# Kernel optimization log

Hardware: AMD Instinct MI355X
Metric: run time of the kernel (lower is better)

The kernel has to match this reference:

```python
import jax, jax.numpy as jnp
import numpy as np

IOU_HI = 0.5
IOU_LO = 0.0
ROI_BS = 256
POS_RATIO = 0.25
BG = 20  # background class id; valid classes 0..BG-1
NUM_POS = int(ROI_BS * POS_RATIO)
DELTAS_SCALING = np.array([10.0, 10.0, 5.0, 5.0], dtype=np.float32)  # (x, y, w, h)


def _make_boxes(key, shape):
    ka, kb = jax.random.split(key)
    c = jax.random.uniform(ka, shape + (2,), minval=0.05, maxval=0.95)
    s = jax.random.uniform(kb, shape + (2,), minval=0.02, maxval=0.4)
    lo = jnp.clip(c - s / 2, 0.0, 1.0)
    hi = jnp.clip(c + s / 2, 0.0, 1.0)
    return jnp.concatenate([lo, hi], -1)  # (y1, x1, y2, x2), normalized


def setup_inputs() -> dict:
    key = jax.random.key(0)
    k1, k2, k3 = jax.random.split(key, 3)
    B, N, G = 32, 12000, 200
    rois = _make_boxes(k1, (B, N))
    gt_boxes = _make_boxes(k2, (B, G))
    # class == BG marks a padded / invalid GT box
    gt_class_ids = jax.random.randint(k3, (B, G), 0, BG + 1).astype(jnp.int32)
    return {"rois": rois, "gt_class_ids": gt_class_ids, "gt_boxes": gt_boxes}


def _iou(rois, gts):
    # rois [N,4], gts [G,4] in (y1,x1,y2,x2) -> [N,G]
    y1 = jnp.maximum(rois[:, None, 0], gts[None, :, 0])
    x1 = jnp.maximum(rois[:, None, 1], gts[None, :, 1])
    y2 = jnp.minimum(rois[:, None, 2], gts[None, :, 2])
    x2 = jnp.minimum(rois[:, None, 3], gts[None, :, 3])
    inter = jnp.clip(y2 - y1, 0.0) * jnp.clip(x2 - x1, 0.0)
    ar = (rois[:, 2] - rois[:, 0]) * (rois[:, 3] - rois[:, 1])
    ag = (gts[:, 2] - gts[:, 0]) * (gts[:, 3] - gts[:, 1])
    return inter / (ar[:, None] + ag[None, :] - inter + 1e-8)


def _encode(r, g):
    # (tx, ty, tw, th) * scaling, r/g: [K,4] in (y1,x1,y2,x2)
    eps = 1e-6
    rh = r[:, 2] - r[:, 0]; rw = r[:, 3] - r[:, 1]
    rcy = r[:, 0] + rh / 2; rcx = r[:, 1] + rw / 2
    gh = g[:, 2] - g[:, 0]; gw = g[:, 3] - g[:, 1]
    gcy = g[:, 0] + gh / 2; gcx = g[:, 1] + gw / 2
    tx = (gcx - rcx) / (rw + eps)
    ty = (gcy - rcy) / (rh + eps)
    tw = jnp.log(jnp.maximum(gw, eps) / (rw + eps))
    th = jnp.log(jnp.maximum(gh, eps) / (rh + eps))
    return jnp.stack([tx, ty, tw, th], -1) * jnp.asarray(DELTAS_SCALING)


def _per_image(rois, gt_cls, gt_boxes):
    iou = _iou(rois, gt_boxes)                       # [N,G]
    valid_gt = gt_cls < BG
    iou = jnp.where(valid_gt[None, :], iou, -1.0)
    max_iou = iou.max(1)                             # [N]
    best_gt = iou.argmax(1)                          # [N]
    pos = max_iou >= IOU_HI
    neg = (max_iou < IOU_HI) & (max_iou >= IOU_LO)

    # deterministic sampling: highest-IoU positives / negatives first
    pos_val, pos_idx = jax.lax.top_k(jnp.where(pos, max_iou, -1.0), NUM_POS)
    pos_ok = pos_val > 0.0
    neg_val, neg_idx = jax.lax.top_k(jnp.where(neg, max_iou + 2.0, -1.0), ROI_BS)
    neg_ok = neg_val > 0.0

    rP = jnp.arange(NUM_POS, dtype=jnp.float32)
    rN = jnp.arange(ROI_BS, dtype=jnp.float32)
    prio = jnp.concatenate([jnp.where(pos_ok, 1e9 - rP, -1e9 - rP),
                            jnp.where(neg_ok, 1e6 - rN, -1e6 - rN)])
    cand_idx = jnp.concatenate([pos_idx, neg_idx])
    cand_pos = jnp.concatenate([pos_ok, jnp.zeros(ROI_BS, bool)])
    _, sel = jax.lax.top_k(prio, ROI_BS)
    sel_roi = cand_idx[sel]                          # [ROI_BS]
    sel_is_pos = cand_pos[sel]                       # [ROI_BS]

    labels = jnp.where(sel_is_pos, gt_cls[best_gt[sel_roi]], BG)
    rois_sel = rois[sel_roi]                         # [ROI_BS,4]
    gts_sel = gt_boxes[best_gt[sel_roi]]             # [ROI_BS,4]
    t = _encode(rois_sel, gts_sel) * sel_is_pos[:, None].astype(rois.dtype)

    cls_onehot = jax.nn.one_hot(labels, BG + 1, dtype=rois.dtype)   # [ROI_BS,BG+1]
    onehot_fg = jax.nn.one_hot(labels, BG, dtype=rois.dtype)        # zero row for bg
    mask4 = jnp.repeat(onehot_fg, 4, axis=1)                        # [ROI_BS,4*BG]
    deltas_full = (onehot_fg[:, :, None] * t[:, None, :]).reshape(ROI_BS, 4 * BG)
    reg = jnp.concatenate([mask4, deltas_full], -1)                 # [ROI_BS,8*BG]
    return rois_sel, cls_onehot, reg


def reference(rois, gt_class_ids, gt_boxes):
    return jax.vmap(_per_image)(rois, gt_class_ids, gt_boxes)
```

## Files before the change

### kernel.cpp

```cpp
#include <hip/hip_runtime.h>
#include <stdint.h>

#pragma clang fp contract(off)

#define BATCH 32
#define NROI  12000
#define NGT   200
#define BGCLS 20
#define ROIBS 256
#define NPOS  64
#define NBIN  1024
#define CAP   1024
#define TSEL  1024
#define VPT2  12
#define HSH   16
#define HST   (NBIN + 2)
#define RPT   2
#define IOBLK (256 * RPT)

__device__ __forceinline__ void roi_maxiou_all(const float4* cbox, const float* carea,
                                               int nv, float ry1, float rx1,
                                               float ry2, float rx2,
                                               float& best, int& bj) {
#pragma clang fp contract(off)
  float ar = (ry2 - ry1) * (rx2 - rx1);
  best = -1.0f; bj = 0;
  for (int j = 0; j < nv; ++j) {
    float4 q = cbox[j];
    float yy1 = fmaxf(ry1, q.x);
    float xx1 = fmaxf(rx1, q.y);
    float yy2 = fminf(ry2, q.z);
    float xx2 = fminf(rx2, q.w);
    float inter = fmaxf(yy2 - yy1, 0.0f) * fmaxf(xx2 - xx1, 0.0f);
    float den = ((ar + carea[j]) - inter) + 1e-8f;
    float iou = inter / den;
    if (iou > best) { best = iou; bj = j; }
  }
}

__global__ __launch_bounds__(256, 4) void k_ioumax(const float* __restrict__ rois,
                                                   const int* __restrict__ gtc,
                                                   const float* __restrict__ gtb,
                                                   float* __restrict__ max_iou,
                                                   int* __restrict__ best_j) {
#pragma clang fp contract(off)
  __shared__ float4 cbox[NGT];
  __shared__ float carea[NGT];
  __shared__ int snv, wtmp[4];
  const int b = blockIdx.y;
  const int tid = threadIdx.x;

  {
    bool valid = false; float4 p = make_float4(0.f, 0.f, 0.f, 0.f);
    if (tid < NGT) {
      p = *(const float4*)(gtb + ((size_t)b * NGT + tid) * 4);
      valid = gtc[(size_t)b * NGT + tid] < BGCLS;
    }
    unsigned long long m = __ballot(valid);
    int w = tid >> 6;
    if ((tid & 63) == 0) wtmp[w] = __popcll(m);
    __syncthreads();
    if (tid == 0) snv = wtmp[0] + wtmp[1] + wtmp[2] + wtmp[3];
    if (valid) {
      int off = 0;
      for (int i = 0; i < w; ++i) off += wtmp[i];
      int pos = off + __popcll(m & ((1ull << (tid & 63)) - 1ull));
      cbox[pos] = p;
      carea[pos] = (p.z - p.x) * (p.w - p.y);
    }
    __syncthreads();
  }
  const int nv = snv;
  const int n0 = blockIdx.x * IOBLK + tid;

  float4 rb[RPT]; float ar[RPT]; float v1[RPT], v2[RPT]; int j1[RPT];
#pragma unroll
  for (int k = 0; k < RPT; ++k) {
    int n = n0 + (k << 8);
    rb[k] = (n < NROI) ? *(const float4*)(rois + ((size_t)b * NROI + n) * 4)
                       : make_float4(2.f, 2.f, 2.f, 2.f);
    ar[k] = (rb[k].z - rb[k].x) * (rb[k].w - rb[k].y);
    v1[k] = -1.0f; v2[k] = -2.0f; j1[k] = 0;
  }
#pragma unroll 2
  for (int j = 0; j < nv; ++j) {
    float4 q = cbox[j];
    float ag = carea[j];
#pragma unroll
    for (int k = 0; k < RPT; ++k) {
      float yy1 = fmaxf(rb[k].x, q.x);
      float xx1 = fmaxf(rb[k].y, q.y);
      float yy2 = fminf(rb[k].z, q.z);
      float xx2 = fminf(rb[k].w, q.w);
      float inter = fmaxf(yy2 - yy1, 0.0f) * fmaxf(xx2 - xx1, 0.0f);
      float den = ((ar[k] + ag) - inter) + 1e-8f;
      float a = inter * __builtin_amdgcn_rcpf(den);
      bool gt = a > v1[k];
      v2[k] = gt ? v1[k] : fmaxf(v2[k], a);
      j1[k] = gt ? j : j1[k];
      v1[k] = gt ? a : v1[k];
    }
  }
#pragma unroll
  for (int k = 0; k < RPT; ++k) {
    int n = n0 + (k << 8);
    if (n >= NROI) continue;
    float best; int bj;
    if (nv == 0) {
      best = -1.0f; bj = 0;
    } else if (v2[k] >= v1[k] * 0.999995f) {
      roi_maxiou_all(cbox, carea, nv, rb[k].x, rb[k].y, rb[k].z, rb[k].w, best, bj);
    } else {
      float4 q = cbox[j1[k]];
      float yy1 = fmaxf(rb[k].x, q.x);
      float xx1 = fmaxf(rb[k].y, q.y);
      float yy2 = fminf(rb[k].z, q.z);
      float xx2 = fminf(rb[k].w, q.w);
      float inter = fmaxf(yy2 - yy1, 0.0f) * fmaxf(xx2 - xx1, 0.0f);
      float den = ((ar[k] + carea[j1[k]]) - inter) + 1e-8f;
      best = inter / den;
      bj = j1[k];
    }
    max_iou[(size_t)b * NROI + n] = best;
    best_j[(size_t)b * NROI + n] = bj;
  }
}

template <bool USE_WS>
__global__ __launch_bounds__(TSEL) void k_sel(const float* __restrict__ rois,
                                              const int* __restrict__ gtc,
                                              const float* __restrict__ gtb,
                                              const float* __restrict__ max_iou,
                                              const int* __restrict__ best_j,
                                              float* __restrict__ out) {
#pragma clang fp contract(off)
  __shared__ float4 cbox[NGT];
  __shared__ float carea[NGT];
  __shared__ int ccls[NGT];
  __shared__ int snv, wtmp[16];
  __shared__ int wtot[16], wnext[16];
  __shared__ unsigned long long list[CAP];
  __shared__ int hs[HSH][HST];
  __shared__ int ss[NBIN];
  __shared__ int sel_r[ROIBS];
  __shared__ int scnt, sT;
  const int b = blockIdx.x;
  const int tid = threadIdx.x;
  const int lane = tid & 63;

  {
    bool valid = false; float4 p = make_float4(0.f, 0.f, 0.f, 0.f); int cls = BGCLS;
    if (tid < NGT) {
      p = *(const float4*)(gtb + ((size_t)b * NGT + tid) * 4);
      cls = gtc[(size_t)b * NGT + tid];
      valid = (cls < BGCLS);
    }
    unsigned long long m = __ballot(valid);
    int w = tid >> 6;
    if ((tid & 63) == 0) wtmp[w] = __popcll(m);
    if (tid < ROIBS) sel_r[tid] = 0;
    __syncthreads();
    if (tid == 0) { int s = 0; for (int i = 0; i < 16; ++i) s += wtmp[i]; snv = s; }
    if (valid) {
      int off = 0;
      for (int i = 0; i < w; ++i) off += wtmp[i];
      int pos = off + __popcll(m & ((1ull << (tid & 63)) - 1ull));
      cbox[pos] = p;
      carea[pos] = (p.z - p.x) * (p.w - p.y);
      ccls[pos] = cls;
    }
    __syncthreads();
  }
  const int nv = snv;

  float v[VPT2];
#pragma unroll
  for (int i = 0; i < VPT2; ++i) {
    int n = tid + (i << 10);
    if constexpr (USE_WS) {
      v[i] = (n < NROI) ? max_iou[(size_t)b * NROI + n] : -3.0f;
    } else {
      if (n < NROI) {
        const float4 r = *(const float4*)(rois + ((size_t)b * NROI + n) * 4);
        float best; int bj;
        roi_maxiou_all(cbox, carea, nv, r.x, r.y, r.z, r.w, best, bj);
        v[i] = best;
      } else v[i] = -3.0f;
    }
  }

  auto phase = [&](bool isPos, int need, unsigned base, int shift,
                   float lo, float hi, int slotBase) -> int {
    for (int i = tid; i < HSH * HST; i += TSEL) ((int*)hs)[i] = 0;
    if (tid == 0) { scnt = 0; sT = 0; }
    __syncthreads();
    const int sh = tid & (HSH - 1);
#pragma unroll
    for (int i = 0; i < VPT2; ++i) {
      float x = v[i];
      if (x >= lo && x < hi) {
        float kv = isPos ? x : (x + 2.0f);
        int bin = min((int)((__float_as_uint(kv) - base) >> shift), NBIN - 1);
        atomicAdd(&hs[sh][bin], 1);
      }
    }
    __syncthreads();
    int cnt_bin = 0;
#pragma unroll
    for (int i = 0; i < HSH; ++i) cnt_bin += hs[i][tid];
    const int w = tid >> 6;
    int sfx = cnt_bin;
#pragma unroll
    for (int off = 1; off < 64; off <<= 1) {
      int t = __shfl_down(sfx, off, 64);
      sfx += (lane + off < 64) ? t : 0;
    }
    if (lane == 0) wtot[w] = sfx;
    __syncthreads();
    if (tid < 16) {
      int s = 0;
      for (int i = tid + 1; i < 16; ++i) s += wtot[i];
      wnext[tid] = s;
    }
    __syncthreads();
    const int suffix = sfx + wnext[w];
    ss[tid] = suffix;
    __syncthreads();
    {
      int nxt = (tid + 1 < NBIN) ? ss[tid + 1] : 0;
      if (suffix >= need && nxt < need) sT = tid;
    }
    __syncthreads();
    const int T = sT;
#pragma unroll
    for (int i = 0; i < VPT2; ++i) {
      int n = tid + (i << 10);
      float x = v[i];
      bool pred = (x >= lo && x < hi);
      unsigned kh = 0; 
      if (pred) {
        kh = __float_as_uint(isPos ? x : (x + 2.0f));
        int bin = min((int)((kh - base) >> shift), NBIN - 1);
        pred = (bin >= T);
      }
      unsigned long long mk = __ballot(pred);
      int c = __popcll(mk);
      int bs = 0;
      if (lane == 0 && c) bs = atomicAdd(&scnt, c);
      bs = __shfl(bs, 0, 64);
      if (pred) {
        int idx = bs + __popcll(mk & ((1ull << lane) - 1ull));
        if (idx < CAP)
          list[idx] = ((unsigned long long)kh << 32) | (unsigned)(0x7fffffff - n);
      }
    }
    __syncthreads();
    const int cnt = min(scnt, CAP);
    const int limit = min(cnt, need);
    if (tid < cnt) {
      unsigned long long ki = list[tid];
      int rank = 0;
      for (int j = 0; j < cnt; ++j) rank += (list[j] > ki);
      if (rank < limit)
        sel_r[slotBase + rank] = 0x7fffffff - (int)(ki & 0xffffffffu);
    }
    __syncthreads();
    return limit;
  };

  const int P = phase(true, NPOS, 0x3F000000u, 13, 0.5f, 3.0f, 0);
  phase(false, ROIBS - P, 0x40000000u, 11, 0.0f, 0.5f, P);

  {
    const int slot = tid >> 2, q = tid & 3;
    const int r = sel_r[slot];
    const int isp = (slot < P) ? 1 : 0;
    const float4 rv = *(const float4*)(rois + ((size_t)b * NROI + r) * 4);
    float ry1 = rv.x, rx1 = rv.y, ry2 = rv.z, rx2 = rv.w;
    int bj;
    if constexpr (USE_WS) {
      bj = best_j[(size_t)b * NROI + r];
    } else {
      float bb;
      roi_maxiou_all(cbox, carea, nv, ry1, rx1, ry2, rx2, bb, bj);
    }
    int label = isp ? ccls[bj] : BGCLS;

    float* out1 = out;
    float* out2 = out + (size_t)BATCH * ROIBS * 4;
    float* out3 = out + (size_t)BATCH * ROIBS * 25;
    size_t row = (size_t)b * ROIBS + slot;

    if (q == 0) {
      *(float4*)(out1 + row * 4) = rv;
      float* o2 = out2 + row * 21;
      for (int c = 0; c <= BGCLS; ++c) o2[c] = (c == label) ? 1.0f : 0.0f;
    }

    float t0 = 0.f, t1 = 0.f, t2 = 0.f, t3 = 0.f;
    if (isp) {
      const float eps = 1e-6f;
      float4 g = cbox[bj];
      float gy1 = g.x, gx1 = g.y, gy2 = g.z, gx2 = g.w;
      float rh = ry2 - ry1, rw = rx2 - rx1;
      float rcy = ry1 + rh * 0.5f, rcx = rx1 + rw * 0.5f;
      float gh = gy2 - gy1, gw = gx2 - gx1;
      float gcy = gy1 + gh * 0.5f, gcx = gx1 + gw * 0.5f;
      t0 = ((gcx - rcx) / (rw + eps)) * 10.0f;
      t1 = ((gcy - rcy) / (rh + eps)) * 10.0f;
      t2 = logf(fmaxf(gw, eps) / (rw + eps)) * 5.0f;
      t3 = logf(fmaxf(gh, eps) / (rh + eps)) * 5.0f;
    }
    int m0 = label * 4;
    float* o3 = out3 + row * 160;
    for (int c = q * 10; c < q * 10 + 10; ++c) {
      float4 wv = make_float4(0.f, 0.f, 0.f, 0.f);
      if (isp) {
        float* wp = &wv.x;
#pragma unroll
        for (int jj = 0; jj < 4; ++jj) {
          int e = c * 4 + jj;
          float x = 0.f;
          if (e >= m0 && e < m0 + 4) x = 1.0f;
          int d = e - 80 - m0;
          if (d == 0) x = t0; else if (d == 1) x = t1;
          else if (d == 2) x = t2; else if (d == 3) x = t3;
          wp[jj] = x;
        }
      }
      *(float4*)(o3 + c * 4) = wv;
    }
  }
}

extern "C" void kernel_launch(void* const* d_in, const int* in_sizes, int n_in,
                              void* d_out, int out_size, void* d_ws, size_t ws_size,
                              hipStream_t stream) {
  const float* rois = (const float*)d_in[0];
  const int*   gtc  = (const int*)d_in[1];
  const float* gtb  = (const float*)d_in[2];
  float*       out  = (float*)d_out;

  size_t need = (size_t)BATCH * NROI * 8;
  if (d_ws && ws_size >= need) {
    float* mi = (float*)d_ws;
    int*   bj = (int*)d_ws + (size_t)BATCH * NROI;
    k_ioumax<<<dim3((NROI + IOBLK - 1) / IOBLK, BATCH), 256, 0, stream>>>(rois, gtc, gtb, mi, bj);
    k_sel<true><<<BATCH, TSEL, 0, stream>>>(rois, gtc, gtb, mi, bj, out);
  } else {
    k_sel<false><<<BATCH, TSEL, 0, stream>>>(rois, gtc, gtb, nullptr, nullptr, out);
  }
}
```

Measured before the change: 89.53 us.

## Use approximate max-IoU prefilter, recompute exact IoU only for boundary candidates

The first kernel now computes only an approximate max IoU per ROI, using a fast reciprocal and a two-way max. It no longer tracks the argmax or runs exact fallbacks, and it stops writing the best_j array. The selection kernel picks candidates with a widened margin around the 0.5 threshold and lowered histogram cutoffs, then recomputes exact IoU and argmax for those candidates only before ranking. This removes the per-ROI argmax bookkeeping and half the workspace traffic. In exchange it adds exact recomputation in the single-block-per-image selection kernel and a larger candidate buffer, and it relies on the margin to keep results exact.

```diff
diff --git a/kernel.cpp b/kernel.cpp
--- a/kernel.cpp
+++ b/kernel.cpp
@@ -10,13 +10,12 @@
 #define ROIBS 256
 #define NPOS  64
 #define NBIN  1024
-#define CAP   1024
+#define CAP   2048
 #define TSEL  1024
 #define VPT2  12
 #define HSH   16
 #define HST   (NBIN + 2)
-#define RPT   2
-#define IOBLK (256 * RPT)
+#define DELTA 1e-6f
 
 __device__ __forceinline__ void roi_maxiou_all(const float4* cbox, const float* carea,
                                                int nv, float ry1, float rx1,
@@ -38,12 +37,29 @@
   }
 }
 
-__global__ __launch_bounds__(256, 4) void k_ioumax(const float* __restrict__ rois,
-                                                   const int* __restrict__ gtc,
-                                                   const float* __restrict__ gtb,
-                                                   float* __restrict__ max_iou,
-                                                   int* __restrict__ best_j) {
-#pragma clang fp contract(off)
+__device__ __forceinline__ float approx_max(const float4* cbox, const float* carea,
+                                            int nv, float4 r) {
+  float ar = (r.z - r.x) * (r.w - r.y);
+  float va = -1.0f, vb = -1.0f;
+#pragma unroll 4
+  for (int j = 0; j < nv; ++j) {
+    float4 q = cbox[j];
+    float yy1 = fmaxf(r.x, q.x);
+    float xx1 = fmaxf(r.y, q.y);
+    float yy2 = fminf(r.z, q.z);
+    float xx2 = fminf(r.w, q.w);
+    float inter = fmaxf(yy2 - yy1, 0.0f) * fmaxf(xx2 - xx1, 0.0f);
+    float den = ((ar + carea[j]) - inter) + 1e-8f;
+    float a = inter * __builtin_amdgcn_rcpf(den);
+    if (j & 1) vb = fmaxf(vb, a); else va = fmaxf(va, a);
+  }
+  return fmaxf(va, vb);
+}
+
+__global__ __launch_bounds__(256) void k_ioumax(const float* __restrict__ rois,
+                                                const int* __restrict__ gtc,
+                                                const float* __restrict__ gtb,
+                                                float* __restrict__ max_iou) {
   __shared__ float4 cbox[NGT];
   __shared__ float carea[NGT];
   __shared__ int snv, wtmp[4];
@@ -70,60 +86,10 @@
     }
     __syncthreads();
   }
-  const int nv = snv;
-  const int n0 = blockIdx.x * IOBLK + tid;
-
-  float4 rb[RPT]; float ar[RPT]; float v1[RPT], v2[RPT]; int j1[RPT];
-#pragma unroll
-  for (int k = 0; k < RPT; ++k) {
-    int n = n0 + (k << 8);
-    rb[k] = (n < NROI) ? *(const float4*)(rois + ((size_t)b * NROI + n) * 4)
-                       : make_float4(2.f, 2.f, 2.f, 2.f);
-    ar[k] = (rb[k].z - rb[k].x) * (rb[k].w - rb[k].y);
-    v1[k] = -1.0f; v2[k] = -2.0f; j1[k] = 0;
-  }
-#pragma unroll 2
-  for (int j = 0; j < nv; ++j) {
-    float4 q = cbox[j];
-    float ag = carea[j];
-#pragma unroll
-    for (int k = 0; k < RPT; ++k) {
-      float yy1 = fmaxf(rb[k].x, q.x);
-      float xx1 = fmaxf(rb[k].y, q.y);
-      float yy2 = fminf(rb[k].z, q.z);
-      float xx2 = fminf(rb[k].w, q.w);
-      float inter = fmaxf(yy2 - yy1, 0.0f) * fmaxf(xx2 - xx1, 0.0f);
-      float den = ((ar[k] + ag) - inter) + 1e-8f;
-      float a = inter * __builtin_amdgcn_rcpf(den);
-      bool gt = a > v1[k];
-      v2[k] = gt ? v1[k] : fmaxf(v2[k], a);
-      j1[k] = gt ? j : j1[k];
-      v1[k] = gt ? a : v1[k];
-    }
-  }
-#pragma unroll
-  for (int k = 0; k < RPT; ++k) {
-    int n = n0 + (k << 8);
-    if (n >= NROI) continue;
-    float best; int bj;
-    if (nv == 0) {
-      best = -1.0f; bj = 0;
-    } else if (v2[k] >= v1[k] * 0.999995f) {
-      roi_maxiou_all(cbox, carea, nv, rb[k].x, rb[k].y, rb[k].z, rb[k].w, best, bj);
-    } else {
-      float4 q = cbox[j1[k]];
-      float yy1 = fmaxf(rb[k].x, q.x);
-      float xx1 = fmaxf(rb[k].y, q.y);
-      float yy2 = fminf(rb[k].z, q.z);
-      float xx2 = fminf(rb[k].w, q.w);
-      float inter = fmaxf(yy2 - yy1, 0.0f) * fmaxf(xx2 - xx1, 0.0f);
-      float den = ((ar[k] + carea[j1[k]]) - inter) + 1e-8f;
-      best = inter / den;
-      bj = j1[k];
-    }
-    max_iou[(size_t)b * NROI + n] = best;
-    best_j[(size_t)b * NROI + n] = bj;
-  }
+  int n = blockIdx.x * 256 + tid;
+  if (n >= NROI) return;
+  const float4 r = *(const float4*)(rois + ((size_t)b * NROI + n) * 4);
+  max_iou[(size_t)b * NROI + n] = approx_max(cbox, carea, snv, r);
 }
 
 template <bool USE_WS>
@@ -131,7 +97,6 @@
                                               const int* __restrict__ gtc,
                                               const float* __restrict__ gtb,
                                               const float* __restrict__ max_iou,
-                                              const int* __restrict__ best_j,
                                               float* __restrict__ out) {
 #pragma clang fp contract(off)
   __shared__ float4 cbox[NGT];
@@ -139,11 +104,14 @@
   __shared__ int ccls[NGT];
   __shared__ int snv, wtmp[16];
   __shared__ int wtot[16], wnext[16];
-  __shared__ unsigned long long list[CAP];
+  __shared__ int plist[CAP];
+  __shared__ unsigned long long keyl[CAP];
+  __shared__ int bjl[CAP];
   __shared__ int hs[HSH][HST];
   __shared__ int ss[NBIN];
   __shared__ int sel_r[ROIBS];
-  __shared__ int scnt, sT;
+  __shared__ int sel_b[ROIBS];
+  __shared__ int scnt, sX, sT, sPos;
   const int b = blockIdx.x;
   const int tid = threadIdx.x;
   const int lane = tid & 63;
@@ -158,7 +126,7 @@
     unsigned long long m = __ballot(valid);
     int w = tid >> 6;
     if ((tid & 63) == 0) wtmp[w] = __popcll(m);
-    if (tid < ROIBS) sel_r[tid] = 0;
+    if (tid < ROIBS) { sel_r[tid] = 0; sel_b[tid] = 0; }
     __syncthreads();
     if (tid == 0) { int s = 0; for (int i = 0; i < 16; ++i) s += wtmp[i]; snv = s; }
     if (valid) {
@@ -177,33 +145,23 @@
 #pragma unroll
   for (int i = 0; i < VPT2; ++i) {
     int n = tid + (i << 10);
-    if constexpr (USE_WS) {
-      v[i] = (n < NROI) ? max_iou[(size_t)b * NROI + n] : -3.0f;
-    } else {
-      if (n < NROI) {
+    if (n < NROI) {
+      if constexpr (USE_WS) {
+        v[i] = max_iou[(size_t)b * NROI + n];
+      } else {
         const float4 r = *(const float4*)(rois + ((size_t)b * NROI + n) * 4);
-        float best; int bj;
-        roi_maxiou_all(cbox, carea, nv, r.x, r.y, r.z, r.w, best, bj);
-        v[i] = best;
-      } else v[i] = -3.0f;
-    }
-  }
-
-  auto phase = [&](bool isPos, int need, unsigned base, int shift,
-                   float lo, float hi, int slotBase) -> int {
-    for (int i = tid; i < HSH * HST; i += TSEL) ((int*)hs)[i] = 0;
-    if (tid == 0) { scnt = 0; sT = 0; }
-    __syncthreads();
-    const int sh = tid & (HSH - 1);
-#pragma unroll
-    for (int i = 0; i < VPT2; ++i) {
-      float x = v[i];
-      if (x >= lo && x < hi) {
-        float kv = isPos ? x : (x + 2.0f);
-        int bin = min((int)((__float_as_uint(kv) - base) >> shift), NBIN - 1);
-        atomicAdd(&hs[sh][bin], 1);
+        v[i] = approx_max(cbox, carea, nv, r);
       }
-    }
+    } else v[i] = -3.0f;
+  }
+
+  auto mkbin = [](unsigned kh, unsigned base, int shift) -> int {
+    int bin = ((int)(kh - base)) >> shift;
+    return max(min(bin, NBIN - 1), 0);
+  };
+
+  auto find_T = [&](int needv) -> int {
+    if (tid == 0) sT = 0;
     __syncthreads();
     int cnt_bin = 0;
 #pragma unroll
@@ -226,64 +184,136 @@
     const int suffix = sfx + wnext[w];
     ss[tid] = suffix;
     __syncthreads();
-    {
-      int nxt = (tid + 1 < NBIN) ? ss[tid + 1] : 0;
-      if (suffix >= need && nxt < need) sT = tid;
-    }
-    __syncthreads();
-    const int T = sT;
-#pragma unroll
-    for (int i = 0; i < VPT2; ++i) {
-      int n = tid + (i << 10);
-      float x = v[i];
-      bool pred = (x >= lo && x < hi);
-      unsigned kh = 0; 
-      if (pred) {
-        kh = __float_as_uint(isPos ? x : (x + 2.0f));
-        int bin = min((int)((kh - base) >> shift), NBIN - 1);
-        pred = (bin >= T);
+    int nxt = (tid + 1 < NBIN) ? ss[tid + 1] : 0;
+    if (suffix >= needv && nxt < needv) sT = tid;
+    __syncthreads();
+    return sT;
+  };
+
+  const int sh = tid & (HSH - 1);
+
+  for (int i = tid; i < HSH * HST; i += TSEL) ((int*)hs)[i] = 0;
+  if (tid == 0) { scnt = 0; sX = 0; sPos = 0; }
+  __syncthreads();
+#pragma unroll
+  for (int i = 0; i < VPT2; ++i) {
+    int n = tid + (i << 10);
+    float x = v[i];
+    bool inb = (n < NROI) && (x >= 0.5f - DELTA);
+    if (inb) atomicAdd(&hs[sh][mkbin(__float_as_uint(x), 0x3F000000u, 13)], 1);
+    bool bnd = inb && (x < 0.5f + DELTA);
+    unsigned long long mx = __ballot(bnd);
+    if (lane == 0 && mx) atomicAdd(&sX, __popcll(mx));
+  }
+  __syncthreads();
+  const int XB = sX;
+  const int Tp = max(find_T(NPOS + XB) - 2, 0);
+#pragma unroll
+  for (int i = 0; i < VPT2; ++i) {
+    int n = tid + (i << 10);
+    float x = v[i];
+    bool pred = (n < NROI) && (x >= 0.5f - DELTA) &&
+                (mkbin(__float_as_uint(x), 0x3F000000u, 13) >= Tp);
+    unsigned long long mk = __ballot(pred);
+    int c = __popcll(mk);
+    int bs = 0;
+    if (lane == 0 && c) bs = atomicAdd(&scnt, c);
+    bs = __shfl(bs, 0, 64);
+    if (pred) {
+      int idx = bs + __popcll(mk & ((1ull << lane) - 1ull));
+      if (idx < CAP) plist[idx] = n;
+    }
+  }
+  __syncthreads();
+  const int cntp = min(scnt, CAP);
+  for (int i = tid; i < cntp; i += TSEL) {
+    int n = plist[i];
+    const float4 r = *(const float4*)(rois + ((size_t)b * NROI + n) * 4);
+    float best; int bj;
+    roi_maxiou_all(cbox, carea, nv, r.x, r.y, r.z, r.w, best, bj);
+    bool ok = (best >= 0.5f);
+    keyl[i] = ok ? (((unsigned long long)__float_as_uint(best) << 32)
+                   | (unsigned)(0x7fffffff - n)) : 0ull;
+    bjl[i] = bj;
+    if (ok) atomicAdd(&sPos, 1);
+  }
+  __syncthreads();
+  const int P = min(sPos, NPOS);
+  for (int i = tid; i < cntp; i += TSEL) {
+    unsigned long long ki = keyl[i];
+    if (ki) {
+      int rank = 0;
+      for (int j = 0; j < cntp; ++j) rank += (keyl[j] > ki);
+      if (rank < P) {
+        sel_r[rank] = 0x7fffffff - (int)(ki & 0xffffffffu);
+        sel_b[rank] = bjl[i];
       }
-      unsigned long long mk = __ballot(pred);
-      int c = __popcll(mk);
-      int bs = 0;
-      if (lane == 0 && c) bs = atomicAdd(&scnt, c);
-      bs = __shfl(bs, 0, 64);
-      if (pred) {
-        int idx = bs + __popcll(mk & ((1ull << lane) - 1ull));
-        if (idx < CAP)
-          list[idx] = ((unsigned long long)kh << 32) | (unsigned)(0x7fffffff - n);
+    }
+  }
+  __syncthreads();
+
+  const int need = ROIBS - P;
+  for (int i = tid; i < HSH * HST; i += TSEL) ((int*)hs)[i] = 0;
+  if (tid == 0) scnt = 0;
+  __syncthreads();
+#pragma unroll
+  for (int i = 0; i < VPT2; ++i) {
+    int n = tid + (i << 10);
+    float x = v[i];
+    if (n < NROI && x < 0.5f + DELTA)
+      atomicAdd(&hs[sh][mkbin(__float_as_uint(x + 2.0f), 0x40000000u, 11)], 1);
+  }
+  __syncthreads();
+  const int Tn = max(find_T(need + XB) - 2, 0);
+#pragma unroll
+  for (int i = 0; i < VPT2; ++i) {
+    int n = tid + (i << 10);
+    float x = v[i];
+    bool pred = (n < NROI) && (x < 0.5f + DELTA) &&
+                (mkbin(__float_as_uint(x + 2.0f), 0x40000000u, 11) >= Tn);
+    unsigned long long mk = __ballot(pred);
+    int c = __popcll(mk);
+    int bs = 0;
+    if (lane == 0 && c) bs = atomicAdd(&scnt, c);
+    bs = __shfl(bs, 0, 64);
+    if (pred) {
+      int idx = bs + __popcll(mk & ((1ull << lane) - 1ull));
+      if (idx < CAP) plist[idx] = n;
+    }
+  }
+  __syncthreads();
+  const int cntn = min(scnt, CAP);
+  for (int i = tid; i < cntn; i += TSEL) {
+    int n = plist[i];
+    const float4 r = *(const float4*)(rois + ((size_t)b * NROI + n) * 4);
+    float best; int bj;
+    roi_maxiou_all(cbox, carea, nv, r.x, r.y, r.z, r.w, best, bj);
+    bool ok = (best < 0.5f);
+    keyl[i] = ok ? (((unsigned long long)__float_as_uint(best + 2.0f) << 32)
+                   | (unsigned)(0x7fffffff - n)) : 0ull;
+    bjl[i] = bj;
+  }
+  __syncthreads();
+  for (int i = tid; i < cntn; i += TSEL) {
+    unsigned long long ki = keyl[i];
+    if (ki) {
+      int rank = 0;
+      for (int j = 0; j < cntn; ++j) rank += (keyl[j] > ki);
+      if (rank < need) {
+        sel_r[P + rank] = 0x7fffffff - (int)(ki & 0xffffffffu);
+        sel_b[P + rank] = bjl[i];
       }
     }
-    __syncthreads();
-    const int cnt = min(scnt, CAP);
-    const int limit = min(cnt, need);
-    if (tid < cnt) {
-      unsigned long long ki = list[tid];
-      int rank = 0;
-      for (int j = 0; j < cnt; ++j) rank += (list[j] > ki);
-      if (rank < limit)
-        sel_r[slotBase + rank] = 0x7fffffff - (int)(ki & 0xffffffffu);
-    }
-    __syncthreads();
-    return limit;
-  };
-
-  const int P = phase(true, NPOS, 0x3F000000u, 13, 0.5f, 3.0f, 0);
-  phase(false, ROIBS - P, 0x40000000u, 11, 0.0f, 0.5f, P);
+  }
+  __syncthreads();
 
   {
     const int slot = tid >> 2, q = tid & 3;
     const int r = sel_r[slot];
+    const int bj = sel_b[slot];
     const int isp = (slot < P) ? 1 : 0;
     const float4 rv = *(const float4*)(rois + ((size_t)b * NROI + r) * 4);
     float ry1 = rv.x, rx1 = rv.y, ry2 = rv.z, rx2 = rv.w;
-    int bj;
-    if constexpr (USE_WS) {
-      bj = best_j[(size_t)b * NROI + r];
-    } else {
-      float bb;
-      roi_maxiou_all(cbox, carea, nv, ry1, rx1, ry2, rx2, bb, bj);
-    }
     int label = isp ? ccls[bj] : BGCLS;
 
     float* out1 = out;
@@ -341,13 +371,12 @@
   const float* gtb  = (const float*)d_in[2];
   float*       out  = (float*)d_out;
 
-  size_t need = (size_t)BATCH * NROI * 8;
+  size_t need = (size_t)BATCH * NROI * sizeof(float);
   if (d_ws && ws_size >= need) {
     float* mi = (float*)d_ws;
-    int*   bj = (int*)d_ws + (size_t)BATCH * NROI;
-    k_ioumax<<<dim3((NROI + IOBLK - 1) / IOBLK, BATCH), 256, 0, stream>>>(rois, gtc, gtb, mi, bj);
-    k_sel<true><<<BATCH, TSEL, 0, stream>>>(rois, gtc, gtb, mi, bj, out);
+    k_ioumax<<<dim3((NROI + 255) / 256, BATCH), 256, 0, stream>>>(rois, gtc, gtb, mi);
+    k_sel<true><<<BATCH, TSEL, 0, stream>>>(rois, gtc, gtb, mi, out);
   } else {
-    k_sel<false><<<BATCH, TSEL, 0, stream>>>(rois, gtc, gtb, nullptr, nullptr, out);
-  }
-}
+    k_sel<false><<<BATCH, TSEL, 0, stream>>>(rois, gtc, gtb, nullptr, out);
+  }
+}
```

Measured after the change: 101.8 us. +13.8%, slower.
